# Kernel optimization log

Measured on AMD Instinct MI355X. Metric: run time of the kernel, lower is better.

## Reference

```python
import jax, jax.numpy as jnp
import numpy as np
from jax import lax

B, T, F_IN = 8, 512, 229
C1 = 48            # model_size_conv // 16
C3 = 96            # model_size_conv // 8
D_CONV = 768       # model_size_conv
D_LSTM = 768       # model_size_lstm
N_PITCH = 88       # MAX_MIDI - MIN_MIDI + 1
N_STATE = 5
EMB = 2
LSTM_IN = D_CONV + N_PITCH * EMB   # 944
FC_IN = C3 * (F_IN // 4)           # 96 * 57 = 5472
BN_EPS = 1e-5


def setup_inputs() -> dict:
    key = jax.random.key(0)
    ks = iter(jax.random.split(key, 64))
    nrm = lambda shape, s=0.05: jax.random.normal(next(ks), shape, jnp.float32) * s
    uni = lambda shape: jax.random.uniform(next(ks), shape, jnp.float32, 0.5, 1.5)
    inp = {
        'mel': jax.random.normal(next(ks), (B, T, F_IN), jnp.float32),
        'conv1_w': nrm((C1, 1, 3, 3)), 'conv1_b': nrm((C1,)),
        'bn1_g': uni((C1,)), 'bn1_b': nrm((C1,)), 'bn1_m': nrm((C1,), 0.1), 'bn1_v': uni((C1,)),
        'conv2_w': nrm((C1, C1, 3, 3)), 'conv2_b': nrm((C1,)),
        'bn2_g': uni((C1,)), 'bn2_b': nrm((C1,)), 'bn2_m': nrm((C1,), 0.1), 'bn2_v': uni((C1,)),
        'conv3_w': nrm((C3, C1, 3, 3)), 'conv3_b': nrm((C3,)),
        'bn3_g': uni((C3,)), 'bn3_b': nrm((C3,)), 'bn3_m': nrm((C3,), 0.1), 'bn3_v': uni((C3,)),
        'fc_w': nrm((D_CONV, FC_IN)), 'fc_b': nrm((D_CONV,)),
        'wih1': nrm((4 * D_LSTM, LSTM_IN)), 'whh1': nrm((4 * D_LSTM, D_LSTM)),
        'bih1': nrm((4 * D_LSTM,)), 'bhh1': nrm((4 * D_LSTM,)),
        'wih2': nrm((4 * D_LSTM, D_LSTM)), 'whh2': nrm((4 * D_LSTM, D_LSTM)),
        'bih2': nrm((4 * D_LSTM,)), 'bhh2': nrm((4 * D_LSTM,)),
        'post_w': nrm((N_PITCH * N_STATE, D_LSTM)), 'post_b': nrm((N_PITCH * N_STATE,)),
        'emb_w': nrm((N_STATE, EMB), 1.0),
    }
    return inp


def _conv_bn_relu(x, w, b, g, be, m, v):
    # x: NCHW, w: OIHW, padding 'SAME' == padding=1 for 3x3
    y = lax.conv_general_dilated(x, w, (1, 1), 'SAME', dimension_numbers=('NCHW', 'OIHW', 'NCHW'))
    y = y + b[None, :, None, None]
    scale = (g / jnp.sqrt(v + BN_EPS))[None, :, None, None]
    y = (y - m[None, :, None, None]) * scale + be[None, :, None, None]
    return jax.nn.relu(y)


def _maxpool12(x):
    # MaxPool2d((1,2)) on NCHW, floor mode
    return lax.reduce_window(x, -jnp.inf, lax.max, (1, 1, 1, 2), (1, 1, 1, 2), 'VALID')


def _lstm_cell(x, h, c, wih, whh, bih, bhh):
    z = x @ wih.T + h @ whh.T + bih + bhh
    i, f, g, o = jnp.split(z, 4, axis=-1)
    c = jax.nn.sigmoid(f) * c + jax.nn.sigmoid(i) * jnp.tanh(g)
    h = jax.nn.sigmoid(o) * jnp.tanh(c)
    return h, c


def _forward(mel, conv1_w, conv1_b, bn1_g, bn1_b, bn1_m, bn1_v,
             conv2_w, conv2_b, bn2_g, bn2_b, bn2_m, bn2_v,
             conv3_w, conv3_b, bn3_g, bn3_b, bn3_m, bn3_v,
             fc_w, fc_b, wih1, whh1, bih1, bhh1, wih2, whh2, bih2, bhh2,
             post_w, post_b, emb_w):
    b = mel.shape[0]
    # --- ConvStack acoustic model (eval mode: dropout = identity) ---
    x = mel[:, None]                                  # (B,1,T,F)
    x = _conv_bn_relu(x, conv1_w, conv1_b, bn1_g, bn1_b, bn1_m, bn1_v)
    x = _conv_bn_relu(x, conv2_w, conv2_b, bn2_g, bn2_b, bn2_m, bn2_v)
    x = _maxpool12(x)
    x = _conv_bn_relu(x, conv3_w, conv3_b, bn3_g, bn3_b, bn3_m, bn3_v)
    x = _maxpool12(x)                                 # (B,C3,T,F//4)
    x = x.transpose(0, 2, 1, 3).reshape(b, -1, FC_IN) # (B,T,C3*F//4)
    acoustic = x @ fc_w.T + fc_b                      # (B,T,768)

    def step(carry, a_t):
        h1, c1, h2, c2, prev = carry                  # prev: (B,88) int32
        emb = emb_w[prev].reshape(prev.shape[0], N_PITCH * EMB)
        xt = jnp.concatenate([a_t, emb], axis=-1)     # (B,944)
        h1n, c1n = _lstm_cell(xt, h1, c1, wih1, whh1, bih1, bhh1)
        h2n, c2n = _lstm_cell(h1n, h2, c2, wih2, whh2, bih2, bhh2)
        logits = (h2n @ post_w.T + post_b).reshape(-1, N_PITCH, N_STATE)
        nprev = jnp.argmax(logits, axis=-1).astype(jnp.int32)  # argmax(softmax)==argmax(logits)
        return (h1n, c1n, h2n, c2n, nprev), logits

    z = jnp.zeros((b, D_LSTM), mel.dtype)
    prev0 = jnp.zeros((b, N_PITCH), jnp.int32)
    _, logits = lax.scan(step, (z, z, z, z, prev0), acoustic.transpose(1, 0, 2))
    return logits.transpose(1, 0, 2, 3)               # (B,T,88,N_STATE)


def reference(mel, conv1_w, conv1_b, bn1_g, bn1_b, bn1_m, bn1_v,
              conv2_w, conv2_b, bn2_g, bn2_b, bn2_m, bn2_v,
              conv3_w, conv3_b, bn3_g, bn3_b, bn3_m, bn3_v,
              fc_w, fc_b, wih1, whh1, bih1, bhh1, wih2, whh2, bih2, bhh2,
              post_w, post_b, emb_w):
    return _forward(mel, conv1_w, conv1_b, bn1_g, bn1_b, bn1_m, bn1_v,
                    conv2_w, conv2_b, bn2_g, bn2_b, bn2_m, bn2_v,
                    conv3_w, conv3_b, bn3_g, bn3_b, bn3_m, bn3_v,
                    fc_w, fc_b, wih1, whh1, bih1, bhh1, wih2, whh2, bih2, bhh2,
                    post_w, post_b, emb_w)
```

## Files before the change

### kernel.cpp

```cpp
#include <hip/hip_runtime.h>
#include <math.h>

#define WS_C3   0u
#define WS_C2CH 22413312u
#define WS_AC   28104192u
#define WS_A1   0u

__device__ __forceinline__ float sigm(float x){ return 1.0f / (1.0f + expf(-x)); }

__device__ __forceinline__ unsigned cloadu(const unsigned* p){
  return __hip_atomic_load(p, __ATOMIC_RELAXED, __HIP_MEMORY_SCOPE_SYSTEM);
}
__device__ __forceinline__ unsigned long long cloadu64(const void* p){
  return __hip_atomic_load((const unsigned long long*)p, __ATOMIC_RELAXED,
                           __HIP_MEMORY_SCOPE_SYSTEM);
}
__device__ __forceinline__ void cstoreu64(void* p, unsigned long long v){
  __hip_atomic_store((unsigned long long*)p, v, __ATOMIC_RELAXED,
                     __HIP_MEMORY_SCOPE_SYSTEM);
}
__device__ __forceinline__ float u2f(unsigned u){
  union { unsigned u; float f; } c; c.u = u; return c.f;
}
__device__ __forceinline__ unsigned f2u(float f){
  union { unsigned u; float f; } c; c.f = f; return c.u;
}

#define SLOT 16
__device__ __forceinline__ void gbar(unsigned* sy, unsigned bar, int wg){
  __syncthreads();
  const int tid = threadIdx.x;
  if (tid == 0)
    __hip_atomic_store(&sy[SLOT + wg*16], bar, __ATOMIC_RELAXED,
                       __HIP_MEMORY_SCOPE_SYSTEM);
  if (tid < 64){
    for (;;){
      unsigned m0 = cloadu(&sy[SLOT + (4*tid + 0)*16]);
      unsigned m1 = cloadu(&sy[SLOT + (4*tid + 1)*16]);
      unsigned m2 = cloadu(&sy[SLOT + (4*tid + 2)*16]);
      unsigned m3 = cloadu(&sy[SLOT + (4*tid + 3)*16]);
      unsigned a = m0 < m1 ? m0 : m1;
      unsigned b = m2 < m3 ? m2 : m3;
      unsigned mn = a < b ? a : b;
      if (__all(mn >= bar)) break;
      __builtin_amdgcn_s_sleep(1);
    }
  }
  __syncthreads();
}

__global__ __launch_bounds__(256) void conv2f_k(
    const float* __restrict__ mel, const float* __restrict__ w1,
    const float* __restrict__ b1, const float* __restrict__ g1,
    const float* __restrict__ be1, const float* __restrict__ m1,
    const float* __restrict__ v1,
    const float* __restrict__ w2, const float* __restrict__ b2,
    const float* __restrict__ g2, const float* __restrict__ be2,
    const float* __restrict__ m2, const float* __restrict__ v2,
    float* __restrict__ c2ch, int t0)
{
  __shared__ float act[3*8*240];
  __shared__ float w2s[48*8*12];
  __shared__ float mel5[5*240];
  __shared__ float w1s[48*12];
  __shared__ float sc1[48], sh1[48], sc2[48], sh2[48];
  int tid = threadIdx.x;
  int b = blockIdx.x / 130, lt = blockIdx.x - b*130;
  int t = t0 - 1 + lt;

  int fg = tid % 29, ocg = tid / 29;
  int f0 = fg * 8, oc0 = ocg * 6;

  if (t < 0 || t > 511){
    if (tid < 232){
      for (int o = 0; o < 6; ++o)
        for (int jj = 0; jj < 4; ++jj){
          int fp = fg*4 + jj;
          if (fp < 114)
            c2ch[((b*48 + oc0 + o)*130 + lt)*114 + fp] = 0.f;
        }
    }
    return;
  }

  for (int idx = tid; idx < 5*240; idx += 256){
    int rr = idx / 240, w = idx - rr*240;
    int tt = t + rr - 2, f = w - 2;
    mel5[idx] = (tt >= 0 && tt < 512 && f >= 0 && f < 229)
                ? mel[(b*512 + tt)*229 + f] : 0.f;
  }
  for (int idx = tid; idx < 48*12; idx += 256){
    int c = idx / 12, q = idx - c*12;
    int kh = q >> 2, kw = q & 3;
    w1s[idx] = (kw < 3) ? w1[c*9 + kh*3 + kw] : 0.f;
  }
  if (tid < 48){
    float s1 = g1[tid] / sqrtf(v1[tid] + 1e-5f);
    sc1[tid] = s1; sh1[tid] = be1[tid] + (b1[tid] - m1[tid]) * s1;
    float s2 = g2[tid] / sqrtf(v2[tid] + 1e-5f);
    sc2[tid] = s2; sh2[tid] = be2[tid] + (b2[tid] - m2[tid]) * s2;
  }

  float acc[6][8];
  #pragma unroll
  for (int o = 0; o < 6; ++o)
    #pragma unroll
    for (int j = 0; j < 8; ++j) acc[o][j] = 0.f;

  for (int ch = 0; ch < 6; ++ch){
    int ci0 = ch * 8;
    __syncthreads();
    for (int idx = tid; idx < 3*8*240; idx += 256){
      int rr = idx / 1920;
      int rem = idx - rr*1920;
      int ci = rem / 240, w = rem - ci*240;
      int tt = t + rr - 1, f = w - 1;
      float val = 0.f;
      if (tt >= 0 && tt < 512 && f >= 0 && f < 229){
        int cg = ci0 + ci;
        float a = 0.f;
        #pragma unroll
        for (int dh = 0; dh < 3; ++dh){
          const float* mr = &mel5[(rr + dh)*240 + w];
          a = fmaf(mr[0], w1s[cg*12 + dh*4 + 0], a);
          a = fmaf(mr[1], w1s[cg*12 + dh*4 + 1], a);
          a = fmaf(mr[2], w1s[cg*12 + dh*4 + 2], a);
        }
        a = a * sc1[cg] + sh1[cg];
        val = a > 0.f ? a : 0.f;
      }
      act[idx] = val;
    }
    for (int idx = tid; idx < 48*8*12; idx += 256){
      int oc = idx / 96;
      int rem = idx - oc*96;
      int ci = rem / 12, q = rem - ci*12;
      int kh = q >> 2, kw = q & 3;
      w2s[idx] = (kw < 3) ? w2[(oc*48 + ci0 + ci)*9 + kh*3 + kw] : 0.f;
    }
    __syncthreads();
    if (tid < 232){
      for (int ci = 0; ci < 8; ++ci){
        #pragma unroll
        for (int kh = 0; kh < 3; ++kh){
          const float* ap = &act[(kh*8 + ci)*240 + f0];
          float4 A0 = *(const float4*)(ap);
          float4 A1v = *(const float4*)(ap + 4);
          float4 A2 = *(const float4*)(ap + 8);
          float L[12] = {A0.x,A0.y,A0.z,A0.w,A1v.x,A1v.y,A1v.z,A1v.w,A2.x,A2.y,A2.z,A2.w};
          #pragma unroll
          for (int o = 0; o < 6; ++o){
            float4 wv = *(const float4*)&w2s[((oc0 + o)*8 + ci)*12 + kh*4];
            #pragma unroll
            for (int j = 0; j < 8; ++j)
              acc[o][j] = fmaf(L[j+2], wv.z, fmaf(L[j+1], wv.y, fmaf(L[j], wv.x, acc[o][j])));
          }
        }
      }
    }
  }
  __syncthreads();
  if (tid < 232){
    #pragma unroll
    for (int o = 0; o < 6; ++o){
      int oc = oc0 + o;
      float s = sc2[oc], hs = sh2[oc];
      #pragma unroll
      for (int jj = 0; jj < 4; ++jj){
        int fp = fg*4 + jj;
        if (fp < 114){
          float v0 = acc[o][2*jj] * s + hs;   v0 = v0 > 0.f ? v0 : 0.f;
          float v1 = acc[o][2*jj+1] * s + hs; v1 = v1 > 0.f ? v1 : 0.f;
          c2ch[((b*48 + oc)*130 + lt)*114 + fp] = v0 > v1 ? v0 : v1;
        }
      }
    }
  }
}

__global__ __launch_bounds__(256) void conv3_k(
    const float* __restrict__ c2ch, const float* __restrict__ w3,
    const float* __restrict__ b3, const float* __restrict__ g3,
    const float* __restrict__ be3, const float* __restrict__ m3,
    const float* __restrict__ v3, float* __restrict__ c3p, int t0)
{
  __shared__ float act[3*8*128];
  __shared__ float w3s[96*8*12];
  __shared__ float sc[96], sh[96];
  int tid = threadIdx.x;
  int b = blockIdx.x >> 7, tl = blockIdx.x & 127;
  int t = t0 + tl;
  if (tid < 96){
    float s = g3[tid] / sqrtf(v3[tid] + 1e-5f);
    sc[tid] = s; sh[tid] = be3[tid] + (b3[tid] - m3[tid]) * s;
  }
  int fg = tid % 15, ocg = tid / 15;
  int f0 = fg * 8, oc0 = ocg * 6;
  float acc[6][8];
  #pragma unroll
  for (int o = 0; o < 6; ++o)
    #pragma unroll
    for (int j = 0; j < 8; ++j) acc[o][j] = 0.f;

  for (int ch = 0; ch < 6; ++ch){
    int ci0 = ch * 8;
    __syncthreads();
    for (int idx = tid; idx < 3*8*128; idx += 256){
      int rr = idx >> 10;
      int rem = idx & 1023;
      int ci = rem >> 7, w = rem & 127;
      int lt = tl + rr;
      int f = w - 1;
      float val = 0.f;
      if (f >= 0 && f < 114)
        val = c2ch[((b*48 + ci0 + ci)*130 + lt)*114 + f];
      act[idx] = val;
    }
    for (int idx = tid; idx < 96*8*12; idx += 256){
      int oc = idx / 96;
      int rem = idx - oc*96;
      int ci = rem / 12, q = rem - ci*12;
      int kh = q >> 2, kw = q & 3;
      w3s[idx] = (kw < 3) ? w3[(oc*48 + ci0 + ci)*9 + kh*3 + kw] : 0.f;
    }
    __syncthreads();
    if (tid < 240){
      for (int ci = 0; ci < 8; ++ci){
        #pragma unroll
        for (int kh = 0; kh < 3; ++kh){
          const float* ap = &act[(kh*8 + ci)*128 + f0];
          float4 A0 = *(const float4*)(ap);
          float4 A1v = *(const float4*)(ap + 4);
          float4 A2 = *(const float4*)(ap + 8);
          float L[12] = {A0.x,A0.y,A0.z,A0.w,A1v.x,A1v.y,A1v.z,A1v.w,A2.x,A2.y,A2.z,A2.w};
          #pragma unroll
          for (int o = 0; o < 6; ++o){
            float4 wv = *(const float4*)&w3s[((oc0 + o)*8 + ci)*12 + kh*4];
            #pragma unroll
            for (int j = 0; j < 8; ++j)
              acc[o][j] = fmaf(L[j+2], wv.z, fmaf(L[j+1], wv.y, fmaf(L[j], wv.x, acc[o][j])));
          }
        }
      }
    }
  }
  __syncthreads();
  if (tid < 240){
    #pragma unroll
    for (int o = 0; o < 6; ++o){
      int oc = oc0 + o;
      float s = sc[oc], hs = sh[oc];
      #pragma unroll
      for (int jj = 0; jj < 4; ++jj){
        int fp = fg*4 + jj;
        if (fp < 57){
          float v0 = acc[o][2*jj] * s + hs;   v0 = v0 > 0.f ? v0 : 0.f;
          float v1 = acc[o][2*jj+1] * s + hs; v1 = v1 > 0.f ? v1 : 0.f;
          c3p[((b*96 + oc)*512 + t)*57 + fp] = v0 > v1 ? v0 : v1;
        }
      }
    }
  }
}

__global__ __launch_bounds__(256) void gemm_fc_k(
    const float* __restrict__ c3p, const float* __restrict__ fcw,
    const float* __restrict__ fcb, float* __restrict__ ac)
{
  __shared__ float As[16*132];
  __shared__ float Bs[16*132];
  int tid = threadIdx.x;
  int m0 = blockIdx.x * 128, n0 = blockIdx.y * 128;
  int tm = (tid & 15) * 8, tn = (tid >> 4) * 8;
  float acc[8][8];
  #pragma unroll
  for (int i = 0; i < 8; ++i)
    #pragma unroll
    for (int j = 0; j < 8; ++j) acc[i][j] = 0.f;

  for (int k0 = 0; k0 < 5472; k0 += 16){
    __syncthreads();
    #pragma unroll
    for (int i = 0; i < 8; ++i){
      int idx = i*256 + tid;
      int k = idx & 15, mm = idx >> 4;
      int gk = k0 + k;
      int ci = (gk * 36793) >> 21;
      int f  = gk - ci*57;
      int gm = m0 + mm;
      int bb = gm >> 9, tt = gm & 511;
      As[k*132 + mm] = c3p[((bb*96 + ci)*512 + tt)*57 + f];
      Bs[k*132 + mm] = fcw[(n0 + mm)*5472 + gk];
    }
    __syncthreads();
    #pragma unroll
    for (int k = 0; k < 16; ++k){
      const float* arow = &As[k*132 + tm];
      const float* brow = &Bs[k*132 + tn];
      float4 a0 = *(const float4*)arow, a1 = *(const float4*)(arow + 4);
      float4 b0 = *(const float4*)brow, b1 = *(const float4*)(brow + 4);
      float av[8] = {a0.x,a0.y,a0.z,a0.w,a1.x,a1.y,a1.z,a1.w};
      float bv[8] = {b0.x,b0.y,b0.z,b0.w,b1.x,b1.y,b1.z,b1.w};
      #pragma unroll
      for (int i = 0; i < 8; ++i)
        #pragma unroll
        for (int j = 0; j < 8; ++j)
          acc[i][j] = fmaf(av[i], bv[j], acc[i][j]);
    }
  }
  #pragma unroll
  for (int i = 0; i < 8; ++i){
    int gm = m0 + tm + i;
    #pragma unroll
    for (int j = 0; j < 8; ++j){
      int gn = n0 + tn + j;
      ac[gm*768 + gn] = acc[i][j] + fcb[gn];
    }
  }
}

__global__ __launch_bounds__(256) void gemm_a1_k(
    const float* __restrict__ ac, const float* __restrict__ wih1,
    const float* __restrict__ bih1, const float* __restrict__ bhh1,
    float* __restrict__ A1)
{
  __shared__ float As[16*132];
  __shared__ float Bs[16*132];
  int tid = threadIdx.x;
  int m0 = blockIdx.x * 128, n0 = blockIdx.y * 128;
  int tm = (tid & 15) * 8, tn = (tid >> 4) * 8;
  float acc[8][8];
  #pragma unroll
  for (int i = 0; i < 8; ++i)
    #pragma unroll
    for (int j = 0; j < 8; ++j) acc[i][j] = 0.f;

  for (int k0 = 0; k0 < 768; k0 += 16){
    __syncthreads();
    #pragma unroll
    for (int i = 0; i < 8; ++i){
      int idx = i*256 + tid;
      int k = idx & 15, mm = idx >> 4;
      int gk = k0 + k;
      As[k*132 + mm] = ac[(m0 + mm)*768 + gk];
      Bs[k*132 + mm] = wih1[(n0 + mm)*944 + gk];
    }
    __syncthreads();
    #pragma unroll
    for (int k = 0; k < 16; ++k){
      const float* arow = &As[k*132 + tm];
      const float* brow = &Bs[k*132 + tn];
      float4 a0 = *(const float4*)arow, a1 = *(const float4*)(arow + 4);
      float4 b0 = *(const float4*)brow, b1 = *(const float4*)(brow + 4);
      float av[8] = {a0.x,a0.y,a0.z,a0.w,a1.x,a1.y,a1.z,a1.w};
      float bv[8] = {b0.x,b0.y,b0.z,b0.w,b1.x,b1.y,b1.z,b1.w};
      #pragma unroll
      for (int i = 0; i < 8; ++i)
        #pragma unroll
        for (int j = 0; j < 8; ++j)
          acc[i][j] = fmaf(av[i], bv[j], acc[i][j]);
    }
  }
  #pragma unroll
  for (int i = 0; i < 8; ++i){
    int gm = m0 + tm + i;
    int tt = gm & 511, bb = gm >> 9;
    #pragma unroll
    for (int j = 0; j < 8; ++j){
      int gn = n0 + tn + j;
      A1[tt*24576 + gn*8 + bb] = acc[i][j] + bih1[gn] + bhh1[gn];
    }
  }
}

#define S2 772
__global__ __launch_bounds__(256, 1) void rec_k(
    const float* __restrict__ A1,
    const float* __restrict__ whh1, const float* __restrict__ wih1,
    const float* __restrict__ wih2, const float* __restrict__ whh2,
    const float* __restrict__ bih2, const float* __restrict__ bhh2,
    const float* __restrict__ postw, const float* __restrict__ postb,
    const float* __restrict__ embw,
    unsigned long long* __restrict__ xat,
    unsigned long long* __restrict__ hat,
    unsigned* __restrict__ slt, unsigned* __restrict__ sy,
    float* __restrict__ out)
{
  const int wg = blockIdx.x, tid = threadIdx.x;
  const int wv = tid >> 6, l = tid & 63;
  __shared__ float xs[8*S2];
  __shared__ float h2s[8*S2];
  __shared__ float cvec[88*5*12];
  __shared__ float zbuf[96];
  __shared__ float red2[160];
  __shared__ unsigned smax[88];

  float wA[12][3];
  float wB[24][3];
  float wC[3][5];
  {
    int Rb = wv*768 + wg*3;
    #pragma unroll
    for (int ki = 0; ki < 12; ++ki){
      int k = l + (ki << 6);
      #pragma unroll
      for (int u = 0; u < 3; ++u)
        wA[ki][u] = whh1[(Rb + u)*768 + k];
    }
    #pragma unroll
    for (int ki = 0; ki < 24; ++ki){
      int k = l + (ki << 6);
      #pragma unroll
      for (int u = 0; u < 3; ++u)
        wB[ki][u] = (k < 768) ? wih2[(Rb + u)*768 + k] : whh2[(Rb + u)*768 + k - 768];
    }
  }
  if (wg < 88){
    #pragma unroll
    for (int kc = 0; kc < 3; ++kc)
      #pragma unroll
      for (int s = 0; s < 5; ++s)
        wC[kc][s] = postw[(wg*5 + s)*768 + tid + (kc << 8)];
  }
  float b2r = 0.f; int fR = 0, fb = 0;
  if (tid < 96){
    int g = tid / 24, rem = tid - g*24;
    int u = rem >> 3; fb = rem & 7;
    fR = g*768 + wg*3 + u;
    b2r = bih2[fR] + bhh2[fR];
  }
  float pbr = (wg < 88 && tid < 40) ? postb[wg*5 + (tid >> 3)] : 0.f;
  float c1r = 0.f, c2r = 0.f;

  for (int idx = tid; idx < 88*5*12; idx += 256){
    int p = idx / 60, rem = idx - p*60;
    int s = rem / 12, r = rem - s*12;
    int g = r / 3, u = r - g*3;
    int row = g*768 + wg*3 + u;
    cvec[idx] = wih1[row*944 + 768 + 2*p]     * embw[s*2]
              + wih1[row*944 + 768 + 2*p + 1] * embw[s*2 + 1];
  }
  for (int idx = tid; idx < 8*S2; idx += 256){ h2s[idx] = 0.f; xs[idx] = 0.f; }
  __syncthreads();

  unsigned bar = 0;

  for (int t = 0; t < 512; ++t){
    const unsigned tg = (unsigned)(t + 1);
    unsigned long long* xb = xat + (size_t)(t & 1) * 6144;
    unsigned long long* hb = hat + (size_t)(t & 1) * 6144;

    float a1v = 0.f;
    if (tid < 96) a1v = A1[t*24576 + fR*8 + fb];

    {
      float acc[3][8];
      #pragma unroll
      for (int u = 0; u < 3; ++u)
        #pragma unroll
        for (int j = 0; j < 8; ++j) acc[u][j] = 0.f;
      #pragma unroll
      for (int ki = 0; ki < 12; ++ki){
        int k = l + (ki << 6);
        float x0 = xs[k],        x1 = xs[S2 + k],   x2 = xs[2*S2 + k], x3 = xs[3*S2 + k];
        float x4 = xs[4*S2 + k], x5 = xs[5*S2 + k], x6 = xs[6*S2 + k], x7 = xs[7*S2 + k];
        #pragma unroll
        for (int u = 0; u < 3; ++u){
          float w = wA[ki][u];
          acc[u][0] = fmaf(w, x0, acc[u][0]);
          acc[u][1] = fmaf(w, x1, acc[u][1]);
          acc[u][2] = fmaf(w, x2, acc[u][2]);
          acc[u][3] = fmaf(w, x3, acc[u][3]);
          acc[u][4] = fmaf(w, x4, acc[u][4]);
          acc[u][5] = fmaf(w, x5, acc[u][5]);
          acc[u][6] = fmaf(w, x6, acc[u][6]);
          acc[u][7] = fmaf(w, x7, acc[u][7]);
        }
      }
      __syncthreads();
      #pragma unroll
      for (int u = 0; u < 3; ++u)
        #pragma unroll
        for (int j = 0; j < 8; ++j){
          float s = acc[u][j];
          s += __shfl_xor(s, 1);  s += __shfl_xor(s, 2);  s += __shfl_xor(s, 4);
          s += __shfl_xor(s, 8);  s += __shfl_xor(s, 16); s += __shfl_xor(s, 32);
          if (l == 0) zbuf[wv*24 + u*8 + j] = s;
        }
      if (wv == 0){
        const unsigned long long* sl =
            (const unsigned long long*)slt + (size_t)(t & 1) * 88 * 8;
        unsigned lo0 = 0, lo1 = 0;
        for (;;){
          unsigned long long v0 = cloadu64(&sl[l*8]);
          unsigned long long v1 = 0xffffffffffffffffull;
          if (l < 24) v1 = cloadu64(&sl[(64 + l)*8]);
          unsigned t0v = (unsigned)(v0 >> 32);
          unsigned t1v = (unsigned)(v1 >> 32);
          unsigned mn = t0v < t1v ? t0v : t1v;
          if (__all(mn >= (unsigned)t)){ lo0 = (unsigned)v0; lo1 = (unsigned)v1; break; }
          __builtin_amdgcn_s_sleep(1);
        }
        smax[l] = lo0;
        if (l < 24) smax[64 + l] = lo1;
      }
      __syncthreads();
      if (tid < 96){
        int g = tid / 24;
        int rowidx = g*3 + ((tid - g*24) >> 3);
        int b = tid & 7;
        float z = zbuf[tid] + a1v;
        for (int p = 0; p < 88; ++p){
          int s = (smax[p] >> (b*4)) & 7;
          z += cvec[(p*5 + s)*12 + rowidx];
        }
        zbuf[tid] = z;
      }
      __syncthreads();
      if (tid < 24){
        float zi = zbuf[tid], zf = zbuf[24 + tid], zg = zbuf[48 + tid], zo = zbuf[72 + tid];
        c1r = sigm(zf)*c1r + sigm(zi)*tanhf(zg);
        float hh = sigm(zo)*tanhf(c1r);
        cstoreu64(&xb[wg*24 + tid],
                  ((unsigned long long)tg << 32) | (unsigned long long)f2u(hh));
      }
      ++bar; gbar(sy, bar, wg);
    }

    {
      unsigned long long av[24];
      #pragma unroll
      for (int i = 0; i < 24; ++i)
        av[i] = cloadu64(&xb[tid + (i << 8)]);
      float acc[3][8];
      #pragma unroll
      for (int u = 0; u < 3; ++u)
        #pragma unroll
        for (int j = 0; j < 8; ++j) acc[u][j] = 0.f;
      #pragma unroll
      for (int ki = 12; ki < 24; ++ki){
        int k = l + ((ki - 12) << 6);
        float x0 = h2s[k],        x1 = h2s[S2 + k],   x2 = h2s[2*S2 + k], x3 = h2s[3*S2 + k];
        float x4 = h2s[4*S2 + k], x5 = h2s[5*S2 + k], x6 = h2s[6*S2 + k], x7 = h2s[7*S2 + k];
        #pragma unroll
        for (int u = 0; u < 3; ++u){
          float w = wB[ki][u];
          acc[u][0] = fmaf(w, x0, acc[u][0]);
          acc[u][1] = fmaf(w, x1, acc[u][1]);
          acc[u][2] = fmaf(w, x2, acc[u][2]);
          acc[u][3] = fmaf(w, x3, acc[u][3]);
          acc[u][4] = fmaf(w, x4, acc[u][4]);
          acc[u][5] = fmaf(w, x5, acc[u][5]);
          acc[u][6] = fmaf(w, x6, acc[u][6]);
          acc[u][7] = fmaf(w, x7, acc[u][7]);
        }
      }
      for (;;){
        bool bad = false;
        #pragma unroll
        for (int i = 0; i < 24; ++i)
          if ((unsigned)(av[i] >> 32) < tg){
            av[i] = cloadu64(&xb[tid + (i << 8)]); bad = true;
          }
        if (!__any(bad)) break;
        __builtin_amdgcn_s_sleep(1);
      }
      #pragma unroll
      for (int i = 0; i < 24; ++i){
        int idx = tid + (i << 8);
        xs[(idx & 7)*S2 + (idx >> 3)] = u2f((unsigned)av[i]);
      }
      __syncthreads();
      #pragma unroll
      for (int ki = 0; ki < 12; ++ki){
        int k = l + (ki << 6);
        float x0 = xs[k],        x1 = xs[S2 + k],   x2 = xs[2*S2 + k], x3 = xs[3*S2 + k];
        float x4 = xs[4*S2 + k], x5 = xs[5*S2 + k], x6 = xs[6*S2 + k], x7 = xs[7*S2 + k];
        #pragma unroll
        for (int u = 0; u < 3; ++u){
          float w = wB[ki][u];
          acc[u][0] = fmaf(w, x0, acc[u][0]);
          acc[u][1] = fmaf(w, x1, acc[u][1]);
          acc[u][2] = fmaf(w, x2, acc[u][2]);
          acc[u][3] = fmaf(w, x3, acc[u][3]);
          acc[u][4] = fmaf(w, x4, acc[u][4]);
          acc[u][5] = fmaf(w, x5, acc[u][5]);
          acc[u][6] = fmaf(w, x6, acc[u][6]);
          acc[u][7] = fmaf(w, x7, acc[u][7]);
        }
      }
      #pragma unroll
      for (int u = 0; u < 3; ++u)
        #pragma unroll
        for (int j = 0; j < 8; ++j){
          float s = acc[u][j];
          s += __shfl_xor(s, 1);  s += __shfl_xor(s, 2);  s += __shfl_xor(s, 4);
          s += __shfl_xor(s, 8);  s += __shfl_xor(s, 16); s += __shfl_xor(s, 32);
          if (l == 0) zbuf[wv*24 + u*8 + j] = s;
        }
      __syncthreads();
      if (tid < 96)
        zbuf[tid] += b2r;
      __syncthreads();
      if (tid < 24){
        float zi = zbuf[tid], zf = zbuf[24 + tid], zg = zbuf[48 + tid], zo = zbuf[72 + tid];
        c2r = sigm(zf)*c2r + sigm(zi)*tanhf(zg);
        float hh = sigm(zo)*tanhf(c2r);
        cstoreu64(&hb[wg*24 + tid],
                  ((unsigned long long)tg << 32) | (unsigned long long)f2u(hh));
      }
    }

    {
      unsigned long long bv[24];
      #pragma unroll
      for (int i = 0; i < 24; ++i)
        bv[i] = cloadu64(&hb[(tid + ((i >> 3) << 8))*8 + (i & 7)]);
      for (;;){
        bool bad = false;
        #pragma unroll
        for (int i = 0; i < 24; ++i)
          if ((unsigned)(bv[i] >> 32) < tg){
            bv[i] = cloadu64(&hb[(tid + ((i >> 3) << 8))*8 + (i & 7)]); bad = true;
          }
        if (!__any(bad)) break;
        __builtin_amdgcn_s_sleep(1);
      }
      float r0[8], r1[8], r2[8];
      #pragma unroll
      for (int q = 0; q < 8; ++q){
        r0[q] = u2f((unsigned)bv[q]);
        r1[q] = u2f((unsigned)bv[8 + q]);
        r2[q] = u2f((unsigned)bv[16 + q]);
      }
      #pragma unroll
      for (int p = 0; p < 8; ++p){
        h2s[p*S2 + tid]       = r0[p];
        h2s[p*S2 + tid + 256] = r1[p];
        h2s[p*S2 + tid + 512] = r2[p];
      }
      if (wg < 88){
        float acc[5][8];
        #pragma unroll
        for (int s = 0; s < 5; ++s)
          #pragma unroll
          for (int j = 0; j < 8; ++j)
            acc[s][j] = fmaf(wC[2][s], r2[j],
                        fmaf(wC[1][s], r1[j], wC[0][s]*r0[j]));
        #pragma unroll
        for (int s = 0; s < 5; ++s)
          #pragma unroll
          for (int j = 0; j < 8; ++j){
            float v = acc[s][j];
            v += __shfl_xor(v, 1);  v += __shfl_xor(v, 2);  v += __shfl_xor(v, 4);
            v += __shfl_xor(v, 8);  v += __shfl_xor(v, 16); v += __shfl_xor(v, 32);
            if (l == 0) red2[(s*8 + j)*4 + wv] = v;
          }
        __syncthreads();
        if (tid < 40){
          float sum = red2[tid*4] + red2[tid*4 + 1] + red2[tid*4 + 2] + red2[tid*4 + 3] + pbr;
          int s = tid >> 3, bb = tid & 7;
          out[bb*225280 + t*440 + wg*5 + s] = sum;
          zbuf[tid] = sum;
        }
        __syncthreads();
        int bs = 0;
        if (tid < 8){
          float best = zbuf[tid];
          #pragma unroll
          for (int s = 1; s < 5; ++s){
            float v = zbuf[s*8 + tid];
            if (v > best){ best = v; bs = s; }
          }
        }
        if (wv == 0){
          unsigned lo = 0;
          #pragma unroll
          for (int b = 0; b < 8; ++b)
            lo |= (unsigned)(__shfl(bs, b) & 7) << (4*b);
          if (l == 0){
            unsigned long long pv =
                ((unsigned long long)tg << 32) | (unsigned long long)lo;
            cstoreu64((unsigned long long*)slt + ((size_t)((t + 1) & 1)*88 + wg)*8, pv);
          }
        }
      }
    }
  }
}

extern "C" void kernel_launch(void* const* d_in, const int* in_sizes, int n_in,
                              void* d_out, int out_size, void* d_ws, size_t ws_size,
                              hipStream_t stream)
{
  (void)in_sizes; (void)n_in; (void)out_size; (void)ws_size;
  const float* mel  = (const float*)d_in[0];
  const float* w1   = (const float*)d_in[1];
  const float* b1   = (const float*)d_in[2];
  const float* g1   = (const float*)d_in[3];
  const float* be1  = (const float*)d_in[4];
  const float* m1   = (const float*)d_in[5];
  const float* v1   = (const float*)d_in[6];
  const float* w2   = (const float*)d_in[7];
  const float* b2   = (const float*)d_in[8];
  const float* g2   = (const float*)d_in[9];
  const float* be2  = (const float*)d_in[10];
  const float* m2   = (const float*)d_in[11];
  const float* v2   = (const float*)d_in[12];
  const float* w3   = (const float*)d_in[13];
  const float* b3   = (const float*)d_in[14];
  const float* g3   = (const float*)d_in[15];
  const float* be3  = (const float*)d_in[16];
  const float* m3   = (const float*)d_in[17];
  const float* v3   = (const float*)d_in[18];
  const float* fcw  = (const float*)d_in[19];
  const float* fcb  = (const float*)d_in[20];
  const float* wih1 = (const float*)d_in[21];
  const float* whh1 = (const float*)d_in[22];
  const float* bih1 = (const float*)d_in[23];
  const float* bhh1 = (const float*)d_in[24];
  const float* wih2 = (const float*)d_in[25];
  const float* whh2 = (const float*)d_in[26];
  const float* bih2 = (const float*)d_in[27];
  const float* bhh2 = (const float*)d_in[28];
  const float* postw= (const float*)d_in[29];
  const float* postb= (const float*)d_in[30];
  const float* embw = (const float*)d_in[31];

  float* ws    = (float*)d_ws;
  float* c3p   = ws + WS_C3;
  float* c2ch  = ws + WS_C2CH;
  float* ac    = ws + WS_AC;
  float* A1    = ws + WS_A1;
  float* st    = ws + WS_AC;
  unsigned long long* xat = (unsigned long long*)st;
  unsigned long long* hat = (unsigned long long*)(st + 24576);
  unsigned* slt = (unsigned*)(st + 49152);
  unsigned* sy  = (unsigned*)(st + 51968);
  float* outp  = (float*)d_out;

  for (int c = 0; c < 4; ++c){
    int t0 = c * 128;
    conv2f_k<<<dim3(8*130), dim3(256), 0, stream>>>(
        mel, w1, b1, g1, be1, m1, v1, w2, b2, g2, be2, m2, v2, c2ch, t0);
    conv3_k<<<dim3(8*128), dim3(256), 0, stream>>>(
        c2ch, w3, b3, g3, be3, m3, v3, c3p, t0);
  }
  gemm_fc_k<<<dim3(32, 6), dim3(256), 0, stream>>>(c3p, fcw, fcb, ac);
  gemm_a1_k<<<dim3(32, 24), dim3(256), 0, stream>>>(ac, wih1, bih1, bhh1, A1);

  hipMemsetAsync(st, 0, 56080 * sizeof(float), stream);

  rec_k<<<dim3(256), dim3(256), 0, stream>>>(
      A1, whh1, wih1, wih2, whh2, bih2, bhh2, postw, postb, embw,
      xat, hat, slt, sy, outp);
}
```

Measured before the change: 22.32 ms.

## Replace all-to-all barrier polling with master-gather flag broadcast and untagged layer-1 exchange

The grid barrier now has only workgroup 255 poll all 256 arrival slots. It then writes a per-workgroup release flag, and each other workgroup polls just its own flag instead of every workgroup scanning all slots. The layer-1 hidden-state exchange drops the 64-bit timestamp tags and retry loop, storing plain floats and reading them as 64-bit pairs after the barrier. This relies on barrier ordering for visibility. It cuts polling traffic and the data exchanged, but adds a two-hop barrier latency and depends on relaxed stores being visible once the flag is seen.

```diff
diff --git a/kernel.cpp b/kernel.cpp
--- a/kernel.cpp
+++ b/kernel.cpp
@@ -8,6 +8,17 @@
 
 __device__ __forceinline__ float sigm(float x){ return 1.0f / (1.0f + expf(-x)); }
 
+__device__ __forceinline__ void cstore(float* p, float v){
+  union { float f; unsigned u; } c; c.f = v;
+  __hip_atomic_store((unsigned*)p, c.u, __ATOMIC_RELAXED,
+                     __HIP_MEMORY_SCOPE_SYSTEM);
+}
+__device__ __forceinline__ void cload64(const float* p, float& a, float& b){
+  unsigned long long u = __hip_atomic_load((const unsigned long long*)p,
+                          __ATOMIC_RELAXED, __HIP_MEMORY_SCOPE_SYSTEM);
+  union { unsigned long long u; float f[2]; } c; c.u = u;
+  a = c.f[0]; b = c.f[1];
+}
 __device__ __forceinline__ unsigned cloadu(const unsigned* p){
   return __hip_atomic_load(p, __ATOMIC_RELAXED, __HIP_MEMORY_SCOPE_SYSTEM);
 }
@@ -27,23 +38,34 @@
 }
 
 #define SLOT 16
+#define FLG  4112
 __device__ __forceinline__ void gbar(unsigned* sy, unsigned bar, int wg){
   __syncthreads();
   const int tid = threadIdx.x;
   if (tid == 0)
     __hip_atomic_store(&sy[SLOT + wg*16], bar, __ATOMIC_RELAXED,
                        __HIP_MEMORY_SCOPE_SYSTEM);
-  if (tid < 64){
-    for (;;){
-      unsigned m0 = cloadu(&sy[SLOT + (4*tid + 0)*16]);
-      unsigned m1 = cloadu(&sy[SLOT + (4*tid + 1)*16]);
-      unsigned m2 = cloadu(&sy[SLOT + (4*tid + 2)*16]);
-      unsigned m3 = cloadu(&sy[SLOT + (4*tid + 3)*16]);
-      unsigned a = m0 < m1 ? m0 : m1;
-      unsigned b = m2 < m3 ? m2 : m3;
-      unsigned mn = a < b ? a : b;
-      if (__all(mn >= bar)) break;
-      __builtin_amdgcn_s_sleep(1);
+  if (wg == 255){
+    if (tid < 64){
+      for (;;){
+        unsigned m0 = cloadu(&sy[SLOT + (4*tid + 0)*16]);
+        unsigned m1 = cloadu(&sy[SLOT + (4*tid + 1)*16]);
+        unsigned m2 = cloadu(&sy[SLOT + (4*tid + 2)*16]);
+        unsigned m3 = cloadu(&sy[SLOT + (4*tid + 3)*16]);
+        unsigned a = m0 < m1 ? m0 : m1;
+        unsigned b = m2 < m3 ? m2 : m3;
+        unsigned mn = a < b ? a : b;
+        if (__all(mn >= bar)) break;
+        __builtin_amdgcn_s_sleep(1);
+      }
+    }
+    __syncthreads();
+    __hip_atomic_store(&sy[FLG + tid*16], bar, __ATOMIC_RELAXED,
+                       __HIP_MEMORY_SCOPE_SYSTEM);
+  } else {
+    if (tid == 0){
+      while (cloadu(&sy[FLG + wg*16]) < bar)
+        __builtin_amdgcn_s_sleep(1);
     }
   }
   __syncthreads();
@@ -381,8 +403,7 @@
     const float* __restrict__ bih2, const float* __restrict__ bhh2,
     const float* __restrict__ postw, const float* __restrict__ postb,
     const float* __restrict__ embw,
-    unsigned long long* __restrict__ xat,
-    unsigned long long* __restrict__ hat,
+    float* __restrict__ xbuf, unsigned long long* __restrict__ hat,
     unsigned* __restrict__ slt, unsigned* __restrict__ sy,
     float* __restrict__ out)
 {
@@ -447,7 +468,7 @@
 
   for (int t = 0; t < 512; ++t){
     const unsigned tg = (unsigned)(t + 1);
-    unsigned long long* xb = xat + (size_t)(t & 1) * 6144;
+    float* xn = xbuf + (t & 1) * 6144;
     unsigned long long* hb = hat + (size_t)(t & 1) * 6144;
 
     float a1v = 0.f;
@@ -521,17 +542,18 @@
         float zi = zbuf[tid], zf = zbuf[24 + tid], zg = zbuf[48 + tid], zo = zbuf[72 + tid];
         c1r = sigm(zf)*c1r + sigm(zi)*tanhf(zg);
         float hh = sigm(zo)*tanhf(c1r);
-        cstoreu64(&xb[wg*24 + tid],
-                  ((unsigned long long)tg << 32) | (unsigned long long)f2u(hh));
+        cstore(&xn[wg*24 + tid], hh);
       }
       ++bar; gbar(sy, bar, wg);
     }
 
     {
-      unsigned long long av[24];
-      #pragma unroll
-      for (int i = 0; i < 24; ++i)
-        av[i] = cloadu64(&xb[tid + (i << 8)]);
+      float sa[12], sb[12];
+      #pragma unroll
+      for (int i = 0; i < 12; ++i){
+        int idx = tid + (i << 8);
+        cload64(xn + 2*idx, sa[i], sb[i]);
+      }
       float acc[3][8];
       #pragma unroll
       for (int u = 0; u < 3; ++u)
@@ -555,20 +577,12 @@
           acc[u][7] = fmaf(w, x7, acc[u][7]);
         }
       }
-      for (;;){
-        bool bad = false;
-        #pragma unroll
-        for (int i = 0; i < 24; ++i)
-          if ((unsigned)(av[i] >> 32) < tg){
-            av[i] = cloadu64(&xb[tid + (i << 8)]); bad = true;
-          }
-        if (!__any(bad)) break;
-        __builtin_amdgcn_s_sleep(1);
-      }
-      #pragma unroll
-      for (int i = 0; i < 24; ++i){
+      #pragma unroll
+      for (int i = 0; i < 12; ++i){
         int idx = tid + (i << 8);
-        xs[(idx & 7)*S2 + (idx >> 3)] = u2f((unsigned)av[i]);
+        int k = idx >> 2, p = (idx & 3) << 1;
+        xs[p*S2 + k]       = sa[i];
+        xs[(p + 1)*S2 + k] = sb[i];
       }
       __syncthreads();
       #pragma unroll
@@ -733,10 +747,10 @@
   float* ac    = ws + WS_AC;
   float* A1    = ws + WS_A1;
   float* st    = ws + WS_AC;
-  unsigned long long* xat = (unsigned long long*)st;
-  unsigned long long* hat = (unsigned long long*)(st + 24576);
-  unsigned* slt = (unsigned*)(st + 49152);
-  unsigned* sy  = (unsigned*)(st + 51968);
+  float* xbuf  = st;
+  unsigned long long* hat = (unsigned long long*)(st + 12288);
+  unsigned* slt = (unsigned*)(st + 36864);
+  unsigned* sy  = (unsigned*)(st + 39680);
   float* outp  = (float*)d_out;
 
   for (int c = 0; c < 4; ++c){
@@ -749,9 +763,9 @@
   gemm_fc_k<<<dim3(32, 6), dim3(256), 0, stream>>>(c3p, fcw, fcb, ac);
   gemm_a1_k<<<dim3(32, 24), dim3(256), 0, stream>>>(ac, wih1, bih1, bhh1, A1);
 
-  hipMemsetAsync(st, 0, 56080 * sizeof(float), stream);
+  hipMemsetAsync(st, 0, 47888 * sizeof(float), stream);
 
   rec_k<<<dim3(256), dim3(256), 0, stream>>>(
       A1, whh1, wih1, wih2, whh2, bih2, bhh2, postw, postb, embw,
-      xat, hat, slt, sy, outp);
-}
+      xbuf, hat, slt, sy, outp);
+}
```

Result: no change. 22.01 ms (-1.4%).
